# Kernel tuning notes

Hardware: AMD Instinct MI355X
Metric: run time of the kernel (lower is better)

Reference implementation:

```python
import jax, jax.numpy as jnp
import numpy as np

NUM_HEADS = 8
NUM_GROUPS = 32
EPS = 1e-5

def group_norm(x, w, b):
    # x: [B, C, L]
    B, C, L = x.shape
    xg = x.reshape(B, NUM_GROUPS, C // NUM_GROUPS, L)
    mean = xg.mean(axis=(2, 3), keepdims=True)
    var = xg.var(axis=(2, 3), keepdims=True)
    xg = (xg - mean) * jax.lax.rsqrt(var + EPS)
    return xg.reshape(B, C, L) * w[None, :, None] + b[None, :, None]

def setup_inputs() -> dict:
    key = jax.random.key(0)
    ks = jax.random.split(key, 5)
    B, C, H, W = 16, 512, 32, 32
    x = jax.random.normal(ks[0], (B, C, H, W), dtype=jnp.float32)
    norm_w = jnp.ones((C,), dtype=jnp.float32)
    norm_b = jnp.zeros((C,), dtype=jnp.float32)
    w_qkv = jax.random.normal(ks[1], (3 * C, C), dtype=jnp.float32) * (1.0 / np.sqrt(C))
    b_qkv = jax.random.normal(ks[2], (3 * C,), dtype=jnp.float32) * 0.02
    w_proj = jax.random.normal(ks[3], (C, C), dtype=jnp.float32) * (1.0 / np.sqrt(C))
    b_proj = jax.random.normal(ks[4], (C,), dtype=jnp.float32) * 0.02
    return {"x": x, "norm_w": norm_w, "norm_b": norm_b, "w_qkv": w_qkv,
            "b_qkv": b_qkv, "w_proj": w_proj, "b_proj": b_proj}

def reference(x, norm_w, norm_b, w_qkv, b_qkv, w_proj, b_proj):
    B, C = x.shape[0], x.shape[1]
    L = int(np.prod(x.shape[2:]))
    xf = x.reshape(B, C, L)
    h = group_norm(xf, norm_w, norm_b)
    # 1x1 conv == channel matmul: [3C, C] x [B, C, L] -> [B, 3C, L]
    qkv = jnp.einsum('oc,bcl->bol', w_qkv, h) + b_qkv[None, :, None]
    ch = C // NUM_HEADS
    qkv = qkv.reshape(B * NUM_HEADS, 3 * ch, L)
    q, k, v = qkv[:, :ch], qkv[:, ch:2 * ch], qkv[:, 2 * ch:]
    scale = 1.0 / np.sqrt(np.sqrt(ch))
    weight = jnp.einsum('bct,bcs->bts', q * scale, k * scale)  # [B*H, L, L]
    weight = jax.nn.softmax(weight.astype(jnp.float32), axis=-1).astype(weight.dtype)
    a = jnp.einsum('bts,bcs->bct', weight, v)  # [B*H, ch, L]
    a = a.reshape(B, C, L)
    out = jnp.einsum('oc,bcl->bol', w_proj, a) + b_proj[None, :, None]
    return out  # [B, C, L]
```

## Files before the change

kernel.cpp:

```cpp
#include <hip/hip_runtime.h>
#include <math.h>


typedef _Float16 f16x8 __attribute__((ext_vector_type(8)));
typedef _Float16 f16x4 __attribute__((ext_vector_type(4)));
typedef float f32x4 __attribute__((ext_vector_type(4)));

#define MFMA_K16(A, B, C) __builtin_amdgcn_mfma_f32_16x16x16f16(A, B, C, 0, 0, 0)

__device__ __forceinline__ void async_cp16(const void* g, void* l) {
  __builtin_amdgcn_global_load_lds(
      (const __attribute__((address_space(1))) void*)g,
      (__attribute__((address_space(3))) void*)l, 16, 0, 0);
}

__global__ __launch_bounds__(256) void cvt_weights(
    const float* __restrict__ wq, const float* __restrict__ wp,
    _Float16* __restrict__ dq, _Float16* __restrict__ dp) {
  int i = blockIdx.x * 256 + threadIdx.x;
  if (i < 196608) {
    float4 v = ((const float4*)wq)[i];
    f16x4 o = {(_Float16)v.x, (_Float16)v.y, (_Float16)v.z, (_Float16)v.w};
    *(f16x4*)&dq[(size_t)i * 4] = o;
  } else {
    int j = i - 196608;
    float4 v = ((const float4*)wp)[j];
    f16x4 o = {(_Float16)v.x, (_Float16)v.y, (_Float16)v.z, (_Float16)v.w};
    *(f16x4*)&dp[(size_t)j * 4] = o;
  }
}

__global__ __launch_bounds__(256) void gn_kernel(
    const float* __restrict__ x, const float* __restrict__ gw,
    const float* __restrict__ gb, _Float16* __restrict__ hT) {
  const int b = blockIdx.x >> 5;
  const int g = blockIdx.x & 31;
  const size_t base = ((size_t)(b * 512 + g * 16)) * 1024;
  const float4* xp = (const float4*)(x + base);
  const int tid = threadIdx.x;

  float4 vals[16];
  float s = 0.f, sq = 0.f;
#pragma unroll
  for (int r = 0; r < 16; ++r) {
    float4 v = xp[tid + 256 * r];
    vals[r] = v;
    s += v.x + v.y + v.z + v.w;
    sq += v.x * v.x + v.y * v.y + v.z * v.z + v.w * v.w;
  }
  __shared__ float rs[256];
  __shared__ float rq[256];
  rs[tid] = s;
  rq[tid] = sq;
  __syncthreads();
  for (int off = 128; off > 0; off >>= 1) {
    if (tid < off) {
      rs[tid] += rs[tid + off];
      rq[tid] += rq[tid + off];
    }
    __syncthreads();
  }
  const float mean = rs[0] * (1.f / 16384.f);
  const float var = rq[0] * (1.f / 16384.f) - mean * mean;
  const float rinv = rsqrtf(var + 1e-5f);
#pragma unroll
  for (int r = 0; r < 16; ++r) {
    const int c = g * 16 + r;
    const float wc = gw[c] * rinv;
    const float bc = gb[c] - mean * wc;
    vals[r].x = vals[r].x * wc + bc;
    vals[r].y = vals[r].y * wc + bc;
    vals[r].z = vals[r].z * wc + bc;
    vals[r].w = vals[r].w * wc + bc;
  }
  _Float16* hb = hT + ((size_t)b * 1024 + tid * 4) * 512 + g * 16;
#pragma unroll
  for (int li = 0; li < 4; ++li) {
    f16x8 o0, o1;
#pragma unroll
    for (int r = 0; r < 8; ++r) {
      float v0 = li == 0 ? vals[r].x : li == 1 ? vals[r].y
                 : li == 2 ? vals[r].z : vals[r].w;
      float v1 = li == 0 ? vals[8 + r].x : li == 1 ? vals[8 + r].y
                 : li == 2 ? vals[8 + r].z : vals[8 + r].w;
      o0[r] = (_Float16)v0;
      o1[r] = (_Float16)v1;
    }
    *(f16x8*)(hb + (size_t)li * 512) = o0;
    *(f16x8*)(hb + (size_t)li * 512 + 8) = o1;
  }
}

template <typename OutT, bool BIAS_ON_M>
__global__ __launch_bounds__(256) void gemm_tn(
    const _Float16* __restrict__ A, const _Float16* __restrict__ B,
    const float* __restrict__ bias, OutT* __restrict__ Out,
    int M, int N, int K, long sA, long sB) {
  __shared__ __align__(16) char smem[34816];
  _Float16* As = (_Float16*)smem;
  _Float16* Bs = As + 128 * 64;
  const int tid = threadIdx.x;
  const int w = tid >> 6, lane = tid & 63;
  const int lx = lane & 15, quad = lane >> 4;
  const int wm = w >> 1, wn = w & 1;
  const int bn = blockIdx.x * 128, bm = blockIdx.y * 128;
  const int z = blockIdx.z;

  const int srow = w * 32 + (lane >> 3);
  const int scol = (((lane & 7) ^ ((lane >> 3) & 7)) * 8);
  const _Float16* Ag = A + (size_t)z * sA + (size_t)(bm + srow) * K + scol;
  const _Float16* Bg = B + (size_t)z * sB + (size_t)(bn + srow) * K + scol;

  f32x4 acc[4][4];
#pragma unroll
  for (int i = 0; i < 4; ++i)
#pragma unroll
    for (int j = 0; j < 4; ++j) acc[i][j] = (f32x4){0.f, 0.f, 0.f, 0.f};

  const int xa = lx & 7;

  for (int k0 = 0; k0 < K; k0 += 64) {
    __syncthreads();
#pragma unroll
    for (int j = 0; j < 4; ++j) {
      async_cp16(Ag + (size_t)j * 8 * K + k0, &As[(w * 32 + j * 8) * 64]);
      async_cp16(Bg + (size_t)j * 8 * K + k0, &Bs[(w * 32 + j * 8) * 64]);
    }
    __syncthreads();
#pragma unroll
    for (int h = 0; h < 2; ++h) {
      f16x8 af[4], bf[4];
#pragma unroll
      for (int mt = 0; mt < 4; ++mt)
        af[mt] = *(const f16x8*)&As[(wm * 64 + mt * 16 + lx) * 64 +
                                    ((h * 4 + quad) ^ xa) * 8];
#pragma unroll
      for (int nt = 0; nt < 4; ++nt)
        bf[nt] = *(const f16x8*)&Bs[(wn * 64 + nt * 16 + lx) * 64 +
                                    ((h * 4 + quad) ^ xa) * 8];
#pragma unroll
      for (int mt = 0; mt < 4; ++mt)
#pragma unroll
        for (int nt = 0; nt < 4; ++nt)
          acc[mt][nt] = __builtin_amdgcn_mfma_f32_16x16x32_f16(
              af[mt], bf[nt], acc[mt][nt], 0, 0, 0);
    }
  }
  __syncthreads();

  OutT* Ob = Out + (size_t)z * M * N;
  if constexpr (sizeof(OutT) == 2) {
    _Float16* T = (_Float16*)smem;
#pragma unroll
    for (int mt = 0; mt < 4; ++mt) {
      const int m0 = bm + wm * 64 + mt * 16 + quad * 4;
      float bm4[4];
#pragma unroll
      for (int i = 0; i < 4; ++i) bm4[i] = BIAS_ON_M ? bias[m0 + i] : 0.f;
#pragma unroll
      for (int nt = 0; nt < 4; ++nt) {
        const int nl = wn * 64 + nt * 16 + lx;
        const float bn1 = BIAS_ON_M ? 0.f : bias[bn + nl];
        f16x4 o = {(_Float16)(acc[mt][nt][0] + (BIAS_ON_M ? bm4[0] : bn1)),
                   (_Float16)(acc[mt][nt][1] + (BIAS_ON_M ? bm4[1] : bn1)),
                   (_Float16)(acc[mt][nt][2] + (BIAS_ON_M ? bm4[2] : bn1)),
                   (_Float16)(acc[mt][nt][3] + (BIAS_ON_M ? bm4[3] : bn1))};
        *(f16x4*)&T[nl * 136 + wm * 64 + mt * 16 + quad * 4] = o;
      }
    }
    __syncthreads();
#pragma unroll
    for (int j = 0; j < 8; ++j) {
      const int r = j * 16 + (tid >> 4), slot = tid & 15;
      f16x8 vv = *(const f16x8*)&T[r * 136 + slot * 8];
      *(f16x8*)((_Float16*)Ob + (size_t)(bn + r) * M + bm + slot * 8) = vv;
    }
  } else {
    float* T32 = (float*)smem;
#pragma unroll
    for (int p = 0; p < 2; ++p) {
      __syncthreads();
      if (wn == p) {
#pragma unroll
        for (int mt = 0; mt < 4; ++mt) {
          const int m0 = bm + wm * 64 + mt * 16 + quad * 4;
          float bm4[4];
#pragma unroll
          for (int i = 0; i < 4; ++i) bm4[i] = BIAS_ON_M ? bias[m0 + i] : 0.f;
#pragma unroll
          for (int nt = 0; nt < 4; ++nt) {
            const int nl = nt * 16 + lx;
            const float bn1 = BIAS_ON_M ? 0.f : bias[bn + p * 64 + nl];
            float4 o = {acc[mt][nt][0] + (BIAS_ON_M ? bm4[0] : bn1),
                        acc[mt][nt][1] + (BIAS_ON_M ? bm4[1] : bn1),
                        acc[mt][nt][2] + (BIAS_ON_M ? bm4[2] : bn1),
                        acc[mt][nt][3] + (BIAS_ON_M ? bm4[3] : bn1)};
            *(float4*)&T32[nl * 136 + wm * 64 + mt * 16 + quad * 4] = o;
          }
        }
      }
      __syncthreads();
#pragma unroll
      for (int j = 0; j < 8; ++j) {
        const int r = j * 8 + (tid >> 5), slot = tid & 31;
        float4 vv = *(const float4*)&T32[r * 136 + slot * 4];
        *(float4*)((float*)Ob + (size_t)(bn + p * 64 + r) * M + bm + slot * 4) =
            vv;
      }
    }
  }
}

#define LQ 72
#define LV 70
#define QSCALE 0.18033688011112042f

__global__ __launch_bounds__(256) void attn_mfma(
    const _Float16* __restrict__ qkvT, _Float16* __restrict__ aT) {
  __shared__ __align__(16) _Float16 ks[64 * LQ];
  __shared__ __align__(16) _Float16 vs[64 * LV];

  const int tid = threadIdx.x;
  const int w = tid >> 6, lane = tid & 63;
  const int lx = lane & 15, quad = lane >> 4;
  const int bh = blockIdx.x, b = bh >> 3, h = bh & 7;
  const int t0 = blockIdx.y * 128;
  const _Float16* qb = qkvT + (size_t)b * 1024 * 1536 + h * 192;

  f16x8 qf[2][2];
#pragma unroll
  for (int g = 0; g < 2; ++g) {
    const _Float16* qrow = qb + (size_t)(t0 + w * 32 + g * 16 + lx) * 1536;
    qf[g][0] = *(const f16x8*)(qrow + quad * 8);
    qf[g][1] = *(const f16x8*)(qrow + 32 + quad * 8);
#pragma unroll
    for (int j = 0; j < 8; ++j) {
      qf[g][0][j] = qf[g][0][j] * (_Float16)QSCALE;
      qf[g][1][j] = qf[g][1][j] * (_Float16)QSCALE;
    }
  }

  const int kr = tid >> 2, kc = (tid & 3) * 16;
  const int vs2 = (tid >> 3) * 2, vc8 = (tid & 7) * 8;
  const _Float16* kgp = qb + (size_t)kr * 1536 + 64 + kc;
  const _Float16* vgp = qb + (size_t)vs2 * 1536 + 128 + vc8;

  f16x8 kp0 = *(const f16x8*)kgp;
  f16x8 kp1 = *(const f16x8*)(kgp + 8);
  f16x8 vp0 = *(const f16x8*)vgp;
  f16x8 vp1 = *(const f16x8*)(vgp + 1536);

  float l_r[2] = {0.f, 0.f};
  f32x4 oacc[2][4];
#pragma unroll
  for (int g = 0; g < 2; ++g)
#pragma unroll
    for (int mt = 0; mt < 4; ++mt) oacc[g][mt] = (f32x4){0.f, 0.f, 0.f, 0.f};

  for (int s0 = 0; s0 < 1024; s0 += 64) {
    __syncthreads();
    *(f16x8*)&ks[kr * LQ + kc] = kp0;
    *(f16x8*)&ks[kr * LQ + kc + 8] = kp1;
#pragma unroll
    for (int i = 0; i < 8; ++i) {
      union { _Float16 hh[2]; unsigned u; } p;
      p.hh[0] = vp0[i];
      p.hh[1] = vp1[i];
      *(unsigned*)&vs[(vc8 + i) * LV + vs2] = p.u;
    }
    __syncthreads();

    if (s0 + 64 < 1024) {
      const _Float16* kg2 = kgp + (size_t)(s0 + 64) * 1536;
      const _Float16* vg2 = vgp + (size_t)(s0 + 64) * 1536;
      kp0 = *(const f16x8*)kg2;
      kp1 = *(const f16x8*)(kg2 + 8);
      vp0 = *(const f16x8*)vg2;
      vp1 = *(const f16x8*)(vg2 + 1536);
    }

    f32x4 sf[2][4];
#pragma unroll
    for (int sb = 0; sb < 4; ++sb) {
      f16x8 k0 = *(const f16x8*)&ks[(sb * 16 + lx) * LQ + quad * 8];
      f16x8 k1 = *(const f16x8*)&ks[(sb * 16 + lx) * LQ + 32 + quad * 8];
#pragma unroll
      for (int g = 0; g < 2; ++g) {
        f32x4 z = {0.f, 0.f, 0.f, 0.f};
        z = __builtin_amdgcn_mfma_f32_16x16x32_f16(k0, qf[g][0], z, 0, 0, 0);
        sf[g][sb] =
            __builtin_amdgcn_mfma_f32_16x16x32_f16(k1, qf[g][1], z, 0, 0, 0);
      }
    }

    f16x4 pf[2][4];
#pragma unroll
    for (int g = 0; g < 2; ++g) {
      float sum = 0.f;
#pragma unroll
      for (int sb = 0; sb < 4; ++sb) {
        float p0 = __builtin_amdgcn_exp2f(sf[g][sb][0]);
        float p1 = __builtin_amdgcn_exp2f(sf[g][sb][1]);
        float p2 = __builtin_amdgcn_exp2f(sf[g][sb][2]);
        float p3 = __builtin_amdgcn_exp2f(sf[g][sb][3]);
        sum += (p0 + p1) + (p2 + p3);
        pf[g][sb] =
            (f16x4){(_Float16)p0, (_Float16)p1, (_Float16)p2, (_Float16)p3};
      }
      l_r[g] += sum;
    }

#pragma unroll
    for (int kb = 0; kb < 4; ++kb)
#pragma unroll
      for (int mt = 0; mt < 4; ++mt) {
        f16x4 vf = *(const f16x4*)&vs[(mt * 16 + lx) * LV + kb * 16 + quad * 4];
        oacc[0][mt] = MFMA_K16(vf, pf[0][kb], oacc[0][mt]);
        oacc[1][mt] = MFMA_K16(vf, pf[1][kb], oacc[1][mt]);
      }
  }

#pragma unroll
  for (int g = 0; g < 2; ++g) {
    float l = l_r[g];
    l += __shfl_xor(l, 16);
    l += __shfl_xor(l, 32);
    const float linv = 1.f / l;
    _Float16* ob =
        aT + ((size_t)b * 1024 + t0 + w * 32 + g * 16 + lx) * 512 + h * 64;
#pragma unroll
    for (int mt = 0; mt < 4; ++mt) {
      f16x4 o = {(_Float16)(oacc[g][mt][0] * linv),
                 (_Float16)(oacc[g][mt][1] * linv),
                 (_Float16)(oacc[g][mt][2] * linv),
                 (_Float16)(oacc[g][mt][3] * linv)};
      *(f16x4*)&ob[mt * 16 + quad * 4] = o;
    }
  }
}

extern "C" void kernel_launch(void* const* d_in, const int* in_sizes, int n_in,
                              void* d_out, int out_size, void* d_ws,
                              size_t ws_size, hipStream_t stream) {
  const float* x = (const float*)d_in[0];
  const float* norm_w = (const float*)d_in[1];
  const float* norm_b = (const float*)d_in[2];
  const float* w_qkv = (const float*)d_in[3];
  const float* b_qkv = (const float*)d_in[4];
  const float* w_proj = (const float*)d_in[5];
  const float* b_proj = (const float*)d_in[6];
  float* out = (float*)d_out;

  _Float16* hT = (_Float16*)d_ws;
  _Float16* qkvT = hT + (size_t)16 * 1024 * 512;
  _Float16* wq = qkvT + (size_t)16 * 1024 * 1536;
  _Float16* wp = wq + (size_t)1536 * 512;
  _Float16* aT = hT;

  cvt_weights<<<1024, 256, 0, stream>>>(w_qkv, w_proj, wq, wp);
  gn_kernel<<<512, 256, 0, stream>>>(x, norm_w, norm_b, hT);
  gemm_tn<_Float16, true><<<dim3(8, 12, 16), 256, 0, stream>>>(
      wq, hT, b_qkv, qkvT, 1536, 1024, 512, 0L, 524288L);
  attn_mfma<<<dim3(128, 8), 256, 0, stream>>>(qkvT, aT);
  gemm_tn<float, false><<<dim3(4, 8, 16), 256, 0, stream>>>(
      aT, wp, b_proj, out, 1024, 512, 512, 524288L, 0L);
}
```

Measured before the change: 203.1 us.

## Stream attention K tiles into double-buffered swizzled LDS via async loads

Moves the K tile in the attention kernel from a register-staged global load plus LDS store to direct global-to-LDS async copies. It double-buffers the K tiles and manually unrolls the key loop by two so the next tile's copy can overlap the current tile's compute. An XOR swizzle replaces the padded row stride to avoid LDS bank conflicts on the MFMA operand reads. In exchange it uses more LDS, and correctness depends on the async copies having completed by the barrier, which relies on implicit vmcnt ordering with the V register loads.

```diff
diff --git a/kernel.cpp b/kernel.cpp
--- a/kernel.cpp
+++ b/kernel.cpp
@@ -211,13 +211,13 @@
   }
 }
 
-#define LQ 72
 #define LV 70
 #define QSCALE 0.18033688011112042f
 
 __global__ __launch_bounds__(256) void attn_mfma(
     const _Float16* __restrict__ qkvT, _Float16* __restrict__ aT) {
-  __shared__ __align__(16) _Float16 ks[64 * LQ];
+  __shared__ __align__(16) _Float16 kb0[64 * 64];
+  __shared__ __align__(16) _Float16 kb1[64 * 64];
   __shared__ __align__(16) _Float16 vs[64 * LV];
 
   const int tid = threadIdx.x;
@@ -240,13 +240,16 @@
     }
   }
 
-  const int kr = tid >> 2, kc = (tid & 3) * 16;
+  const _Float16* kgs = qb + (size_t)(w * 16 + (lane >> 3)) * 1536 + 64 +
+                        (((lane & 7) ^ ((lane >> 3) & 7)) * 8);
+  _Float16* const kld0 = &kb0[(w * 16) * 64];
+  _Float16* const kld1 = &kb1[(w * 16) * 64];
+
   const int vs2 = (tid >> 3) * 2, vc8 = (tid & 7) * 8;
-  const _Float16* kgp = qb + (size_t)kr * 1536 + 64 + kc;
   const _Float16* vgp = qb + (size_t)vs2 * 1536 + 128 + vc8;
 
-  f16x8 kp0 = *(const f16x8*)kgp;
-  f16x8 kp1 = *(const f16x8*)(kgp + 8);
+  async_cp16(kgs, kld0);
+  async_cp16(kgs + (size_t)8 * 1536, kld0 + 8 * 64);
   f16x8 vp0 = *(const f16x8*)vgp;
   f16x8 vp1 = *(const f16x8*)(vgp + 1536);
 
@@ -257,10 +260,10 @@
 #pragma unroll
     for (int mt = 0; mt < 4; ++mt) oacc[g][mt] = (f32x4){0.f, 0.f, 0.f, 0.f};
 
-  for (int s0 = 0; s0 < 1024; s0 += 64) {
-    __syncthreads();
-    *(f16x8*)&ks[kr * LQ + kc] = kp0;
-    *(f16x8*)&ks[kr * LQ + kc + 8] = kp1;
+  const int xa = lx & 7;
+
+  auto tile = [&](int s0, const _Float16* kcur, _Float16* kldn) {
+    __syncthreads();
 #pragma unroll
     for (int i = 0; i < 8; ++i) {
       union { _Float16 hh[2]; unsigned u; } p;
@@ -271,10 +274,9 @@
     __syncthreads();
 
     if (s0 + 64 < 1024) {
-      const _Float16* kg2 = kgp + (size_t)(s0 + 64) * 1536;
+      async_cp16(kgs + (size_t)(s0 + 64) * 1536, kldn);
+      async_cp16(kgs + (size_t)(s0 + 72) * 1536, kldn + 8 * 64);
       const _Float16* vg2 = vgp + (size_t)(s0 + 64) * 1536;
-      kp0 = *(const f16x8*)kg2;
-      kp1 = *(const f16x8*)(kg2 + 8);
       vp0 = *(const f16x8*)vg2;
       vp1 = *(const f16x8*)(vg2 + 1536);
     }
@@ -282,8 +284,9 @@
     f32x4 sf[2][4];
 #pragma unroll
     for (int sb = 0; sb < 4; ++sb) {
-      f16x8 k0 = *(const f16x8*)&ks[(sb * 16 + lx) * LQ + quad * 8];
-      f16x8 k1 = *(const f16x8*)&ks[(sb * 16 + lx) * LQ + 32 + quad * 8];
+      f16x8 k0 = *(const f16x8*)&kcur[(sb * 16 + lx) * 64 + ((quad ^ xa) * 8)];
+      f16x8 k1 =
+          *(const f16x8*)&kcur[(sb * 16 + lx) * 64 + (((4 + quad) ^ xa) * 8)];
 #pragma unroll
       for (int g = 0; g < 2; ++g) {
         f32x4 z = {0.f, 0.f, 0.f, 0.f};
@@ -318,6 +321,11 @@
         oacc[0][mt] = MFMA_K16(vf, pf[0][kb], oacc[0][mt]);
         oacc[1][mt] = MFMA_K16(vf, pf[1][kb], oacc[1][mt]);
       }
+  };
+
+  for (int s0 = 0; s0 < 1024; s0 += 128) {
+    tile(s0, kb0, kld1);
+    tile(s0 + 64, kb1, kld0);
   }
 
 #pragma unroll
```

After: 207.5 us. +2.2%, slower.
